# Kernel tuning notes

Hardware: AMD Instinct MI355X
Metric: run time of the kernel (lower is better)

Reference implementation:

```python
import jax, jax.numpy as jnp
import numpy as np

# GNB per-element parameters [s, beta, R, C6] indexed by atomic number Z (rows not listed stay zero)
_ROWS = {
 1:[0.2772,1.7504,3.6516,95.99], 2:[0.2425,2.087,2.1843,40.67], 3:[0.3266,2.3073,1.2711,70.21],
 4:[0.3964,2.8811,3.3497,114.51], 5:[0.3121,2.6366,2.7079,152.36], 6:[0.2455,3.0189,1.8219,184.28],
 7:[0.2743,2.9432,2.4667,482.54], 8:[0.2577,2.7407,2.365,405.57], 9:[0.2791,2.5863,1.5062,218.45],
 10:[0.2378,2.5307,1.8233,174.81], 11:[0.2592,2.5679,1.3974,181.7], 12:[0.3837,2.9613,3.3515,263.02],
 13:[0.3013,3.2377,3.0102,228.1], 14:[0.3202,3.2749,3.1629,359.43], 15:[0.3399,3.7491,3.2554,3222.12],
 16:[0.3215,3.6718,2.9539,2144.49], 17:[0.3071,3.418,3.0368,2072.46], 18:[0.2752,3.3306,2.6598,1357.42],
 19:[0.2264,2.9736,4.0877,1406.65], 20:[0.4015,3.4464,4.1275,1058.36], 21:[0.9388,4.5955,9.7282,11498.73],
 22:[0.6048,3.5334,8.5322,3361.33], 23:[0.3678,3.068,7.2344,2095.91], 24:[0.2848,2.8393,5.3605,1049.31],
 25:[0.355,3.055,3.718,966.27], 26:[0.4406,3.2628,3.6408,1571.36], 27:[0.4124,3.2622,3.4961,1183.59],
 28:[0.3139,2.749,3.5108,787.76], 29:[0.3345,2.9097,3.0537,563.93], 30:[0.3391,2.9024,3.0261,592.91],
 31:[0.3146,3.3924,3.1735,430.82], 32:[0.3327,3.2804,3.1773,812.57], 33:[0.404,3.8757,3.8357,4533.53],
 34:[0.3343,3.8562,3.1109,3440.92], 35:[0.3242,3.7067,3.2122,3859.82], 36:[0.292,3.6457,2.8263,2729.6],
 37:[0.2677,3.4421,2.412,1864.19], 38:[0.3446,3.559,1.894,1175.73], 39:[1.0038,5.7293,11.2061,32141.18],
 40:[0.6146,5.075,6.821,27655.14], 41:[0.4244,3.7156,7.2367,2864.2], 42:[0.4882,3.6853,3.901,3563.45],
 43:[0.4439,3.6987,4.0857,3266.43], 44:[0.4736,3.7826,4.045,3967.23], 45:[0.4039,3.4706,3.4813,2233.82],
 46:[0.3188,3.3433,3.0487,1393.49], 47:[0.2948,3.1186,2.7795,1315.09], 48:[0.3012,3.0853,2.8673,1311.47],
 49:[0.3351,3.5452,3.3339,1460.56], 50:[0.3134,3.2997,3.0086,1662.99], 51:[0.4081,4.1277,3.9919,8089.97],
 52:[0.3585,4.1795,3.4209,6887.05], 53:[0.3574,4.0988,3.5649,8799.32], 54:[0.3134,4.0387,3.0288,6136.5],
 55:[0.2872,3.8468,2.262,3757.31], 56:[0.3788,4.0368,1.3837,2561.18], 57:[1.0851,6.1365,12.171,66580.83],
 72:[0.5577,5.213,6.0791,27593.76], 73:[0.5308,4.7637,5.7661,15364.65], 74:[0.3926,3.6018,3.6366,2734.5],
 75:[0.5351,3.9552,4.241,4801.82], 76:[0.4701,4.0278,4.1348,5685.94], 77:[0.3661,3.6123,3.4213,2786.0],
 78:[0.3411,3.6066,3.2486,2699.79], 79:[0.3164,3.3822,2.9588,2282.6], 80:[0.3047,3.375,2.9381,2476.79],
 81:[0.2802,3.3964,2.7711,2988.7], 82:[0.2682,3.2481,2.5816,2506.63], 83:[0.3876,4.1225,3.785,8916.84],
 84:[0.3679,4.2313,3.5381,8694.22], 85:[0.368,4.2455,3.6985,11821.61], 86:[0.3195,4.1784,3.0551,8410.64],
}
_TAB = np.zeros((87, 4), np.float32)
for _z, _v in _ROWS.items():
    _TAB[_z] = _v
GNB_TABLE = jnp.asarray(_TAB)
C_SP2 = jnp.asarray(np.array([0.2808, 3.0548, 2.2348, 429.69], np.float32))
C_SP3 = jnp.asarray(np.array([0.2455, 3.0189, 1.8219, 184.28], np.float32))
N_CN2 = jnp.asarray(np.array([0.2996, 3.02, 2.6454, 720.18], np.float32))
N_CN3 = jnp.asarray(np.array([0.2743, 2.9432, 2.4667, 482.54], np.float32))

BJ_A1, BJ_A2, BJ_ALPHA = 0.4, 4.0, 14.0
CUTOFF_LR, CUTOFF_START = 10.0, 8.0  # cutoff_start = cutoff_lr - 2.0


def _poly_envelope(x):
    # PolynomialCutoff.calculate_envelope with r_max=1, p=6:
    x6 = x ** 6
    env = 1.0 - 28.0 * x6 + 48.0 * x6 * x - 21.0 * x6 * x * x
    return env * (x < 1.0)


def _gnb_forward(lengths, Z, edge_index):
    n_nodes = Z.shape[0]
    sender, receiver = edge_index[0], edge_index[1]

    # coordination numbers via scatter-add on receiver
    cn = jnp.zeros((n_nodes,), jnp.int32).at[receiver].add(1)

    # species-indexed params with CN-adaptive selection for C and N
    params = GNB_TABLE[Z]  # [N, 4]
    c_params = jnp.where((cn <= 3)[:, None], C_SP2[None, :], C_SP3[None, :])
    n_params = jnp.where((cn <= 2)[:, None], N_CN2[None, :], N_CN3[None, :])
    params = jnp.where((Z == 6)[:, None], c_params, params)
    params = jnp.where((Z == 7)[:, None], n_params, params)

    R_i = params[:, 2]
    C6_i = params[:, 3]

    # geometric-mean combination rules per edge
    C6_ij = jnp.sqrt(C6_i[sender] * C6_i[receiver])
    R_ij = jnp.sqrt(R_i[sender] * R_i[receiver])

    r = lengths
    # BJ damping: f = 1 / (1 + 6 (r/r0)^(-alpha)), r0 = a1 sqrt(R_ij) + a2
    r0 = BJ_A1 * jnp.sqrt(R_ij) + BJ_A2
    f_damp = 1.0 / (1.0 + 6.0 * (r0 / r) ** BJ_ALPHA)

    e_edge = -C6_ij / (R_ij ** 6 + r ** 6) * f_damp

    # long-range polynomial cutoff switching from 1 at cutoff_start to 0 at cutoff_lr
    x = (r - CUTOFF_START) / (CUTOFF_LR - CUTOFF_START)
    env = jnp.where(r < CUTOFF_START, 1.0, _poly_envelope(x))
    e_edge = e_edge * env

    # scatter-sum to atoms; 0.5 to split symmetric pair energy over both directions
    node_energy = jnp.zeros((n_nodes,), e_edge.dtype).at[receiver].add(0.5 * e_edge)
    return node_energy


def setup_inputs() -> dict:
    key = jax.random.key(0)
    k1, k2, k3 = jax.random.split(key, 3)
    n_nodes, n_edges = 100000, 6400000
    Z = jax.random.randint(k1, (n_nodes,), 1, 87, dtype=jnp.int32)
    edge_index = jax.random.randint(k2, (2, n_edges), 0, n_nodes, dtype=jnp.int32)
    lengths = jax.random.uniform(k3, (n_edges,), jnp.float32, 1.0, 10.5)
    return {"Z": Z, "edge_index": edge_index, "lengths": lengths}


def reference(Z, edge_index, lengths):
    return _gnb_forward(lengths, Z, edge_index)
```

## Files before the change

### kernel.cpp

```cpp
#include <hip/hip_runtime.h>


#define B2SHIFT 10
#define B2SIZE  1024
#define TILE    4096
#define SBLK    512
#define ESLICES 32
#define MAXB    128

__device__ __constant__ float2 GNB_RC6[87] = {
    {0.f, 0.f},
    {3.6516f, 95.99f},   {2.1843f, 40.67f},   {1.2711f, 70.21f},
    {3.3497f, 114.51f},  {2.7079f, 152.36f},  {1.8219f, 184.28f},
    {2.4667f, 482.54f},  {2.365f, 405.57f},   {1.5062f, 218.45f},
    {1.8233f, 174.81f},  {1.3974f, 181.7f},   {3.3515f, 263.02f},
    {3.0102f, 228.1f},   {3.1629f, 359.43f},  {3.2554f, 3222.12f},
    {2.9539f, 2144.49f}, {3.0368f, 2072.46f}, {2.6598f, 1357.42f},
    {4.0877f, 1406.65f}, {4.1275f, 1058.36f}, {9.7282f, 11498.73f},
    {8.5322f, 3361.33f}, {7.2344f, 2095.91f}, {5.3605f, 1049.31f},
    {3.718f, 966.27f},   {3.6408f, 1571.36f}, {3.4961f, 1183.59f},
    {3.5108f, 787.76f},  {3.0537f, 563.93f},  {3.0261f, 592.91f},
    {3.1735f, 430.82f},  {3.1773f, 812.57f},  {3.8357f, 4533.53f},
    {3.1109f, 3440.92f}, {3.2122f, 3859.82f}, {2.8263f, 2729.6f},
    {2.412f, 1864.19f},  {1.894f, 1175.73f},  {11.2061f, 32141.18f},
    {6.821f, 27655.14f}, {7.2367f, 2864.2f},  {3.901f, 3563.45f},
    {4.0857f, 3266.43f}, {4.045f, 3967.23f},  {3.4813f, 2233.82f},
    {3.0487f, 1393.49f}, {2.7795f, 1315.09f}, {2.8673f, 1311.47f},
    {3.3339f, 1460.56f}, {3.0086f, 1662.99f}, {3.9919f, 8089.97f},
    {3.4209f, 6887.05f}, {3.5649f, 8799.32f}, {3.0288f, 6136.5f},
    {2.262f, 3757.31f},  {1.3837f, 2561.18f}, {12.171f, 66580.83f},
    {0.f,0.f},{0.f,0.f},{0.f,0.f},{0.f,0.f},{0.f,0.f},{0.f,0.f},{0.f,0.f},
    {0.f,0.f},{0.f,0.f},{0.f,0.f},{0.f,0.f},{0.f,0.f},{0.f,0.f},{0.f,0.f},
    {6.0791f, 27593.76f}, {5.7661f, 15364.65f}, {3.6366f, 2734.5f},
    {4.241f, 4801.82f},   {4.1348f, 5685.94f},  {3.4213f, 2786.0f},
    {3.2486f, 2699.79f},  {2.9588f, 2282.6f},   {2.9381f, 2476.79f},
    {2.7711f, 2988.7f},   {2.5816f, 2506.63f},  {3.785f, 8916.84f},
    {3.5381f, 8694.22f},  {3.6985f, 11821.61f}, {3.0551f, 8410.64f},
};

__global__ void gnb_init(const int* __restrict__ Z, unsigned* __restrict__ isCN,
                         int nw, int n_nodes, int* __restrict__ zp, int zwords) {
    int stride = gridDim.x * blockDim.x;
    int t0 = blockIdx.x * blockDim.x + threadIdx.x;
    for (int i = t0; i < zwords; i += stride) zp[i] = 0;
    for (int w = t0; w < nw; w += stride) {
        unsigned m = 0;
        int base = w << 5;
        int lim = n_nodes - base; if (lim > 32) lim = 32;
        for (int k = 0; k < lim; ++k) {
            int z = Z[base + k];
            if (z == 6 || z == 7) m |= (1u << k);
        }
        isCN[w] = m;
    }
}

__global__ void __launch_bounds__(SBLK)
gnb_scatter(const int* __restrict__ send, const int* __restrict__ recv,
            const float* __restrict__ len, const unsigned* __restrict__ isCN,
            int* __restrict__ cn,
            uint2* __restrict__ buckets, unsigned* __restrict__ cursor,
            uint4* __restrict__ ovrec, unsigned* __restrict__ ocur,
            int n_edges, int cap, unsigned ocap, int NB2) {
    __shared__ unsigned cnt[MAXB];
    __shared__ unsigned pos[MAXB];
    __shared__ unsigned startp[MAXB + 1];
    __shared__ unsigned gbase[MAXB];
    __shared__ uint2 srec[TILE];
    __shared__ unsigned char bmap[TILE];
    const int tid = threadIdx.x;
    const int e0  = blockIdx.x * TILE;

    for (int b = tid; b < MAXB; b += SBLK) { cnt[b] = 0; pos[b] = 0; }
    __syncthreads();

    #pragma unroll
    for (int k = 0; k < 2; ++k) {
        int base = e0 + (k * SBLK + tid) * 4;
        if (base + 3 < n_edges) {
            int4   rv = *(const int4*)(recv + base);
            float4 lv = *(const float4*)(len + base);
            int rr[4] = {rv.x, rv.y, rv.z, rv.w};
            float ll[4] = {lv.x, lv.y, lv.z, lv.w};
            #pragma unroll
            for (int j = 0; j < 4; ++j) {
                unsigned r = (unsigned)rr[j];
                if (ll[j] < 10.0f) atomicAdd(&cnt[r >> B2SHIFT], 1u);
                if ((isCN[r >> 5] >> (r & 31)) & 1u) atomicAdd(&cn[r], 1);
            }
        } else {
            int lim = n_edges - base; if (lim < 0) lim = 0; if (lim > 4) lim = 4;
            for (int j = 0; j < lim; ++j) {
                unsigned r = (unsigned)recv[base + j];
                if (len[base + j] < 10.0f) atomicAdd(&cnt[r >> B2SHIFT], 1u);
                if ((isCN[r >> 5] >> (r & 31)) & 1u) atomicAdd(&cn[r], 1);
            }
        }
    }
    __syncthreads();

    if (tid == 0) {
        unsigned acc = 0;
        for (int b = 0; b < NB2; ++b) { startp[b] = acc; acc += cnt[b]; }
        startp[NB2] = acc;
    }
    __syncthreads();
    if (tid < NB2) gbase[tid] = atomicAdd(&cursor[tid], cnt[tid]);
    __syncthreads();

    #pragma unroll
    for (int k = 0; k < 2; ++k) {
        int base = e0 + (k * SBLK + tid) * 4;
        if (base + 3 < n_edges) {
            int4   sv = *(const int4*)(send + base);
            int4   rv = *(const int4*)(recv + base);
            uint4  lv = *(const uint4*)(len + base);
            int ss[4] = {sv.x, sv.y, sv.z, sv.w};
            int rr[4] = {rv.x, rv.y, rv.z, rv.w};
            unsigned ll[4] = {lv.x, lv.y, lv.z, lv.w};
            #pragma unroll
            for (int j = 0; j < 4; ++j) {
                if (__uint_as_float(ll[j]) >= 10.0f) continue;
                unsigned r = (unsigned)rr[j];
                unsigned b = r >> B2SHIFT;
                unsigned slot = startp[b] + atomicAdd(&pos[b], 1u);
                srec[slot] = make_uint2((unsigned)ss[j] | ((r & (B2SIZE - 1)) << 17), ll[j]);
                bmap[slot] = (unsigned char)b;
            }
        } else {
            int lim = n_edges - base; if (lim < 0) lim = 0; if (lim > 4) lim = 4;
            for (int j = 0; j < lim; ++j) {
                unsigned lbits = ((const unsigned*)len)[base + j];
                if (__uint_as_float(lbits) >= 10.0f) continue;
                unsigned r = (unsigned)recv[base + j];
                unsigned b = r >> B2SHIFT;
                unsigned slot = startp[b] + atomicAdd(&pos[b], 1u);
                srec[slot] = make_uint2((unsigned)send[base + j] | ((r & (B2SIZE - 1)) << 17),
                                        lbits);
                bmap[slot] = (unsigned char)b;
            }
        }
    }
    __syncthreads();

    unsigned total = startp[NB2];
    for (unsigned i = tid; i < total; i += SBLK) {
        unsigned b = bmap[i];
        unsigned g = gbase[b] + (i - startp[b]);
        uint2 rec = srec[i];
        if (g < (unsigned)cap) {
            buckets[(size_t)b * cap + g] = rec;
        } else {
            unsigned o = atomicAdd(ocur, 1u);
            unsigned r = ((unsigned)b << B2SHIFT) | ((rec.x >> 17) & (B2SIZE - 1));
            if (o < ocap) ovrec[o] = make_uint4(r, rec.x & 0x1FFFFu, rec.y, 0u);
        }
    }
}

__global__ void gnb_params(const int* __restrict__ Z, const int* __restrict__ cn,
                           float2* __restrict__ P2, int n_nodes) {
    int i = blockIdx.x * blockDim.x + threadIdx.x;
    if (i >= n_nodes) return;
    int z = Z[i];
    float Rp, C6;
    if (z == 6) {
        if (cn[i] <= 3) { Rp = 2.2348f; C6 = 429.69f; }
        else            { Rp = 1.8219f; C6 = 184.28f; }
    } else if (z == 7) {
        if (cn[i] <= 2) { Rp = 2.6454f; C6 = 720.18f; }
        else            { Rp = 2.4667f; C6 = 482.54f; }
    } else {
        float2 rc = GNB_RC6[z];
        Rp = rc.x; C6 = rc.y;
    }
    P2[i] = make_float2(sqrtf(C6), sqrtf(sqrtf(Rp)));
}

__device__ __forceinline__ float gnb_energy_eval(float2 ps, float2 pr, float rlen) {
    float env;
    if (rlen < 8.0f) {
        env = 1.0f;
    } else {
        float x = (rlen - 8.0f) * 0.5f;
        float x2 = x * x;
        float x6 = x2 * x2 * x2;
        env = 1.0f - 28.0f * x6 + 48.0f * x6 * x - 21.0f * x6 * x2;
    }
    float sR  = ps.y * pr.y;
    float C6  = ps.x * pr.x;
    float Rij = sR * sR;
    float R3  = Rij * Rij * Rij;
    float R6  = R3 * R3;
    float r0  = 0.4f * sR + 4.0f;
    float t   = r0 / rlen;
    float t2 = t * t, t4 = t2 * t2, t8 = t4 * t4;
    float t14 = t8 * t4 * t2;
    float fd = 1.0f / (1.0f + 6.0f * t14);
    float rl2 = rlen * rlen;
    float r6 = rl2 * rl2 * rl2;
    return -0.5f * C6 / (R6 + r6) * fd * env;
}

__global__ void __launch_bounds__(256)
gnb_energy(const uint2* __restrict__ buckets, const unsigned* __restrict__ cursor,
           const float2* __restrict__ P2, float* __restrict__ rep,
           int cap, int n_nodes) {
    __shared__ float  acc[2][B2SIZE + 8];
    __shared__ float2 p2loc[B2SIZE];
    const int b   = blockIdx.x / ESLICES;
    const int sl  = blockIdx.x % ESLICES;
    const int tid = threadIdx.x;
    const int rr  = (tid >> 6) & 1;

    for (int i = tid; i < 2 * (B2SIZE + 8); i += 256) acc[0][i] = 0.0f;
    for (int i = tid; i < B2SIZE; i += 256) {
        int node = (b << B2SHIFT) + i;
        p2loc[i] = (node < n_nodes) ? P2[node] : make_float2(0.f, 0.f);
    }
    __syncthreads();

    unsigned count = cursor[b];
    if (count > (unsigned)cap) count = (unsigned)cap;
    unsigned seg = (count + ESLICES - 1) / ESLICES;
    unsigned st  = (unsigned)sl * seg;
    unsigned en  = st + seg; if (en > count) en = count;

    const uint2* src = buckets + (size_t)b * cap;
    for (unsigned i = st + tid; i < en; i += 256) {
        uint2 rec = src[i];
        unsigned s    = rec.x & 0x1FFFFu;
        unsigned rlow = (rec.x >> 17) & (B2SIZE - 1);
        float e = gnb_energy_eval(P2[s], p2loc[rlow], __uint_as_float(rec.y));
        atomicAdd(&acc[rr][rlow], e);
    }
    __syncthreads();

    float* dst = rep + (size_t)blockIdx.x * B2SIZE;
    for (int i = tid; i < B2SIZE; i += 256) dst[i] = acc[0][i] + acc[1][i];
}

__global__ void gnb_ovf_energy(const uint4* __restrict__ ovrec, const unsigned* __restrict__ ocur,
                               const float2* __restrict__ P2, float* __restrict__ ovf,
                               unsigned ocap) {
    unsigned n = *ocur; if (n > ocap) n = ocap;
    int stride = gridDim.x * blockDim.x;
    for (unsigned i = blockIdx.x * blockDim.x + threadIdx.x; i < n; i += stride) {
        uint4 rec = ovrec[i];
        float rlen = __uint_as_float(rec.z);
        if (rlen >= 10.0f) continue;
        float e = gnb_energy_eval(P2[rec.y], P2[rec.x], rlen);
        atomicAdd(&ovf[rec.x], e);
    }
}

__global__ void gnb_reduce(const float* __restrict__ rep, const float* __restrict__ ovf,
                           float* __restrict__ out, int n_nodes) {
    int i = blockIdx.x * blockDim.x + threadIdx.x;
    if (i >= n_nodes) return;
    int b = i >> B2SHIFT;
    int j = i & (B2SIZE - 1);
    const float* src = rep + ((size_t)b * ESLICES) * B2SIZE + j;
    float sum = ovf[i];
    #pragma unroll
    for (int s = 0; s < ESLICES; ++s) sum += src[(size_t)s * B2SIZE];
    out[i] = sum;
}

extern "C" void kernel_launch(void* const* d_in, const int* in_sizes, int n_in,
                              void* d_out, int out_size, void* d_ws, size_t ws_size,
                              hipStream_t stream) {
    const int*   Z    = (const int*)d_in[0];
    const int*   eidx = (const int*)d_in[1];
    const float* len  = (const float*)d_in[2];
    float*       out  = (float*)d_out;

    const int n_nodes = in_sizes[0];
    const int n_edges = in_sizes[2];
    const int* send = eidx;
    const int* recv = eidx + n_edges;

    const int NB2 = (n_nodes + B2SIZE - 1) >> B2SHIFT;
    const int nw  = (n_nodes + 31) >> 5;
    const int nwp = (nw + 7) & ~7;

    char* ws = (char*)d_ws;
    unsigned* cursor = (unsigned*)ws;
    unsigned* ocur   = (unsigned*)(ws + MAXB * 4);
    int*      cn     = (int*)(ws + (MAXB + 8) * 4);
    float*    ovf    = (float*)(ws + ((size_t)n_nodes + MAXB + 8) * 4);
    float2*   P2     = (float2*)(ws + ((size_t)2 * n_nodes + MAXB + 8) * 4);
    unsigned* isCN   = (unsigned*)(ws + ((size_t)4 * n_nodes + MAXB + 8) * 4);
    float*    rep    = (float*)((char*)isCN + (size_t)nwp * 4);
    size_t rep_w     = (size_t)NB2 * ESLICES * B2SIZE;
    char*     tail   = (char*)rep + rep_w * 4;

    size_t fixed_words = (size_t)4 * n_nodes + MAXB + 8 + nwp + rep_w;
    size_t total_words = ws_size / 4;
    size_t avail = total_words > fixed_words ? total_words - fixed_words : 0;
    size_t ovw = avail / 32;
    unsigned ocap = (unsigned)(ovw / 4);
    long cap = (long)((avail - ovw) / (2 * (size_t)NB2));
    if (cap > n_edges) cap = n_edges;
    if (cap < 0) cap = 0;
    uint4* ovrec   = (uint4*)tail;
    uint2* buckets = (uint2*)(tail + (size_t)ocap * 16);

    const int B = 256;
    int node_blocks = (n_nodes + B - 1) / B;
    int scat_blocks = (n_edges + TILE - 1) / TILE;
    int zero_words  = 2 * n_nodes + MAXB + 8;

    gnb_init<<<256, B, 0, stream>>>(Z, isCN, nw, n_nodes, (int*)ws, zero_words);
    gnb_scatter<<<scat_blocks, SBLK, 0, stream>>>(send, recv, len, isCN, cn, buckets,
                                                  cursor, ovrec, ocur, n_edges,
                                                  (int)cap, ocap, NB2);
    gnb_params<<<node_blocks, B, 0, stream>>>(Z, cn, P2, n_nodes);
    gnb_energy<<<NB2 * ESLICES, B, 0, stream>>>(buckets, cursor, P2, rep, (int)cap, n_nodes);
    gnb_ovf_energy<<<8, B, 0, stream>>>(ovrec, ocur, P2, ovf, ocap);
    gnb_reduce<<<node_blocks, B, 0, stream>>>(rep, ovf, out, n_nodes);
}
```

Baseline: 203.2 us.

## Fuse overflow and reduction into energy kernel, use byte param ids

The per-node float2 parameter array is replaced by a one-byte parameter id per node plus a 91-entry table. The table is built in the init kernel and staged in shared memory by the energy kernel, so the random sender gathers shrink from 8 bytes to 1 byte. The energy kernel now uses 16 slices instead of 32 and reads two records per thread with 128-bit loads. A last-block-done counter per bucket lets the final slice process that bucket's overflow records and write the summed output, which removes the separate overflow and reduce launches. In exchange, the last block of each bucket scans the whole overflow list, and fewer slices per bucket means less parallelism.

```diff
diff --git a/kernel.cpp b/kernel.cpp
--- a/kernel.cpp
+++ b/kernel.cpp
@@ -5,7 +5,7 @@
 #define B2SIZE  1024
 #define TILE    4096
 #define SBLK    512
-#define ESLICES 32
+#define ES      16
 #define MAXB    128
 
 __device__ __constant__ float2 GNB_RC6[87] = {
@@ -39,7 +39,8 @@
 };
 
 __global__ void gnb_init(const int* __restrict__ Z, unsigned* __restrict__ isCN,
-                         int nw, int n_nodes, int* __restrict__ zp, int zwords) {
+                         float2* __restrict__ PT, int nw, int n_nodes,
+                         int* __restrict__ zp, int zwords) {
     int stride = gridDim.x * blockDim.x;
     int t0 = blockIdx.x * blockDim.x + threadIdx.x;
     for (int i = t0; i < zwords; i += stride) zp[i] = 0;
@@ -52,6 +53,15 @@
             if (z == 6 || z == 7) m |= (1u << k);
         }
         isCN[w] = m;
+    }
+    if (t0 < 91) {
+        float R, C6;
+        if      (t0 < 87)  { float2 rc = GNB_RC6[t0]; R = rc.x; C6 = rc.y; }
+        else if (t0 == 87) { R = 2.2348f; C6 = 429.69f; }
+        else if (t0 == 88) { R = 1.8219f; C6 = 184.28f; }
+        else if (t0 == 89) { R = 2.6454f; C6 = 720.18f; }
+        else               { R = 2.4667f; C6 = 482.54f; }
+        PT[t0] = make_float2(sqrtf(C6), sqrtf(sqrtf(R)));
     }
 }
 
@@ -159,22 +169,14 @@
 }
 
 __global__ void gnb_params(const int* __restrict__ Z, const int* __restrict__ cn,
-                           float2* __restrict__ P2, int n_nodes) {
+                           unsigned char* __restrict__ pid, int n_nodes) {
     int i = blockIdx.x * blockDim.x + threadIdx.x;
     if (i >= n_nodes) return;
     int z = Z[i];
-    float Rp, C6;
-    if (z == 6) {
-        if (cn[i] <= 3) { Rp = 2.2348f; C6 = 429.69f; }
-        else            { Rp = 1.8219f; C6 = 184.28f; }
-    } else if (z == 7) {
-        if (cn[i] <= 2) { Rp = 2.6454f; C6 = 720.18f; }
-        else            { Rp = 2.4667f; C6 = 482.54f; }
-    } else {
-        float2 rc = GNB_RC6[z];
-        Rp = rc.x; C6 = rc.y;
-    }
-    P2[i] = make_float2(sqrtf(C6), sqrtf(sqrtf(Rp)));
+    int id = z;
+    if (z == 6)      id = (cn[i] <= 3) ? 87 : 88;
+    else if (z == 7) id = (cn[i] <= 2) ? 89 : 90;
+    pid[i] = (unsigned char)id;
 }
 
 __device__ __forceinline__ float gnb_energy_eval(float2 ps, float2 pr, float rlen) {
@@ -204,67 +206,89 @@
 
 __global__ void __launch_bounds__(256)
 gnb_energy(const uint2* __restrict__ buckets, const unsigned* __restrict__ cursor,
-           const float2* __restrict__ P2, float* __restrict__ rep,
-           int cap, int n_nodes) {
+           const float2* __restrict__ PT, const unsigned char* __restrict__ pid,
+           float* __restrict__ rep, unsigned* __restrict__ done,
+           const uint4* __restrict__ ovrec, const unsigned* __restrict__ ocur,
+           float* __restrict__ out, unsigned ocap, int cap, int n_nodes) {
     __shared__ float  acc[2][B2SIZE + 8];
     __shared__ float2 p2loc[B2SIZE];
-    const int b   = blockIdx.x / ESLICES;
-    const int sl  = blockIdx.x % ESLICES;
+    __shared__ float2 ptab[96];
+    __shared__ unsigned s_old;
     const int tid = threadIdx.x;
+    const int b   = blockIdx.x / ES;
+    const int sl  = blockIdx.x % ES;
     const int rr  = (tid >> 6) & 1;
 
+    if (tid < 91) ptab[tid] = PT[tid];
     for (int i = tid; i < 2 * (B2SIZE + 8); i += 256) acc[0][i] = 0.0f;
     for (int i = tid; i < B2SIZE; i += 256) {
         int node = (b << B2SHIFT) + i;
-        p2loc[i] = (node < n_nodes) ? P2[node] : make_float2(0.f, 0.f);
+        p2loc[i] = (node < n_nodes) ? PT[pid[node]] : make_float2(0.f, 0.f);
     }
     __syncthreads();
 
     unsigned count = cursor[b];
     if (count > (unsigned)cap) count = (unsigned)cap;
-    unsigned seg = (count + ESLICES - 1) / ESLICES;
+    unsigned seg = (((count + ES - 1) / ES) + 1) & ~1u;
     unsigned st  = (unsigned)sl * seg;
     unsigned en  = st + seg; if (en > count) en = count;
 
     const uint2* src = buckets + (size_t)b * cap;
-    for (unsigned i = st + tid; i < en; i += 256) {
-        uint2 rec = src[i];
-        unsigned s    = rec.x & 0x1FFFFu;
-        unsigned rlow = (rec.x >> 17) & (B2SIZE - 1);
-        float e = gnb_energy_eval(P2[s], p2loc[rlow], __uint_as_float(rec.y));
-        atomicAdd(&acc[rr][rlow], e);
+    for (unsigned i = st + 2 * tid; i < en; i += 512) {
+        if (i + 1 < en) {
+            uint4 q = *(const uint4*)(src + i);
+            {
+                unsigned s = q.x & 0x1FFFFu, rl = (q.x >> 17) & (B2SIZE - 1);
+                float e = gnb_energy_eval(ptab[pid[s]], p2loc[rl], __uint_as_float(q.y));
+                atomicAdd(&acc[rr][rl], e);
+            }
+            {
+                unsigned s = q.z & 0x1FFFFu, rl = (q.z >> 17) & (B2SIZE - 1);
+                float e = gnb_energy_eval(ptab[pid[s]], p2loc[rl], __uint_as_float(q.w));
+                atomicAdd(&acc[rr][rl], e);
+            }
+        } else {
+            uint2 rec = src[i];
+            unsigned s = rec.x & 0x1FFFFu, rl = (rec.x >> 17) & (B2SIZE - 1);
+            float e = gnb_energy_eval(ptab[pid[s]], p2loc[rl], __uint_as_float(rec.y));
+            atomicAdd(&acc[rr][rl], e);
+        }
     }
     __syncthreads();
 
     float* dst = rep + (size_t)blockIdx.x * B2SIZE;
     for (int i = tid; i < B2SIZE; i += 256) dst[i] = acc[0][i] + acc[1][i];
-}
-
-__global__ void gnb_ovf_energy(const uint4* __restrict__ ovrec, const unsigned* __restrict__ ocur,
-                               const float2* __restrict__ P2, float* __restrict__ ovf,
-                               unsigned ocap) {
-    unsigned n = *ocur; if (n > ocap) n = ocap;
-    int stride = gridDim.x * blockDim.x;
-    for (unsigned i = blockIdx.x * blockDim.x + threadIdx.x; i < n; i += stride) {
-        uint4 rec = ovrec[i];
-        float rlen = __uint_as_float(rec.z);
-        if (rlen >= 10.0f) continue;
-        float e = gnb_energy_eval(P2[rec.y], P2[rec.x], rlen);
-        atomicAdd(&ovf[rec.x], e);
-    }
-}
-
-__global__ void gnb_reduce(const float* __restrict__ rep, const float* __restrict__ ovf,
-                           float* __restrict__ out, int n_nodes) {
-    int i = blockIdx.x * blockDim.x + threadIdx.x;
-    if (i >= n_nodes) return;
-    int b = i >> B2SHIFT;
-    int j = i & (B2SIZE - 1);
-    const float* src = rep + ((size_t)b * ESLICES) * B2SIZE + j;
-    float sum = ovf[i];
-    #pragma unroll
-    for (int s = 0; s < ESLICES; ++s) sum += src[(size_t)s * B2SIZE];
-    out[i] = sum;
+
+    __threadfence();
+    if (tid == 0) s_old = atomicAdd(&done[b], 1u);
+    __syncthreads();
+    if (s_old != ES - 1) return;
+    __threadfence();
+
+    {
+        unsigned n = *ocur; if (n > ocap) n = ocap;
+        for (unsigned i = tid; i < n; i += 256) {
+            uint4 rec = ovrec[i];
+            if ((int)(rec.x >> B2SHIFT) != b) continue;
+            float rlen = __uint_as_float(rec.z);
+            if (rlen >= 10.0f) continue;
+            float e = gnb_energy_eval(ptab[pid[rec.y]], p2loc[rec.x & (B2SIZE - 1)], rlen);
+            atomicAdd(&acc[0][rec.x & (B2SIZE - 1)], e);
+        }
+    }
+    __syncthreads();
+
+    const float* base = rep + ((size_t)b * ES) * B2SIZE;
+    for (int i = tid; i < B2SIZE; i += 256) {
+        int node = (b << B2SHIFT) + i;
+        if (node >= n_nodes) continue;
+        float sum = acc[0][i] - (acc[0][i] + acc[1][i]);
+        sum = 0.0f;
+        #pragma unroll
+        for (int s = 0; s < ES; ++s) sum += base[(size_t)s * B2SIZE + i];
+        sum += (acc[0][i] + acc[1][i]) - dst[i];
+        out[node] = sum;
+    }
 }
 
 extern "C" void kernel_launch(void* const* d_in, const int* in_sizes, int n_in,
@@ -282,41 +306,49 @@
 
     const int NB2 = (n_nodes + B2SIZE - 1) >> B2SHIFT;
     const int nw  = (n_nodes + 31) >> 5;
-    const int nwp = (nw + 7) & ~7;
+    const size_t nwp   = ((size_t)nw + 3) & ~3ull;
+    const size_t npidw = (((size_t)n_nodes + 3) / 4 + 3) & ~3ull;
+
+    size_t o_done = 136;
+    size_t o_cn   = 264;
+    size_t o_PT   = o_cn + n_nodes;
+    size_t o_isCN = o_PT + 192;
+    size_t o_pid  = o_isCN + nwp;
+    size_t o_rep  = (o_pid + npidw + 3) & ~3ull;
+    size_t rep_w  = (size_t)NB2 * ES * B2SIZE;
+    size_t o_tail = (o_rep + rep_w + 3) & ~3ull;
 
     char* ws = (char*)d_ws;
-    unsigned* cursor = (unsigned*)ws;
-    unsigned* ocur   = (unsigned*)(ws + MAXB * 4);
-    int*      cn     = (int*)(ws + (MAXB + 8) * 4);
-    float*    ovf    = (float*)(ws + ((size_t)n_nodes + MAXB + 8) * 4);
-    float2*   P2     = (float2*)(ws + ((size_t)2 * n_nodes + MAXB + 8) * 4);
-    unsigned* isCN   = (unsigned*)(ws + ((size_t)4 * n_nodes + MAXB + 8) * 4);
-    float*    rep    = (float*)((char*)isCN + (size_t)nwp * 4);
-    size_t rep_w     = (size_t)NB2 * ESLICES * B2SIZE;
-    char*     tail   = (char*)rep + rep_w * 4;
-
-    size_t fixed_words = (size_t)4 * n_nodes + MAXB + 8 + nwp + rep_w;
+    unsigned*      cursor = (unsigned*)ws;
+    unsigned*      ocur   = (unsigned*)(ws + 128 * 4);
+    unsigned*      done   = (unsigned*)(ws + o_done * 4);
+    int*           cn     = (int*)(ws + o_cn * 4);
+    float2*        PT     = (float2*)(ws + o_PT * 4);
+    unsigned*      isCN   = (unsigned*)(ws + o_isCN * 4);
+    unsigned char* pid    = (unsigned char*)(ws + o_pid * 4);
+    float*         rep    = (float*)(ws + o_rep * 4);
+
     size_t total_words = ws_size / 4;
-    size_t avail = total_words > fixed_words ? total_words - fixed_words : 0;
+    size_t avail = total_words > o_tail ? total_words - o_tail : 0;
     size_t ovw = avail / 32;
     unsigned ocap = (unsigned)(ovw / 4);
     long cap = (long)((avail - ovw) / (2 * (size_t)NB2));
     if (cap > n_edges) cap = n_edges;
     if (cap < 0) cap = 0;
-    uint4* ovrec   = (uint4*)tail;
-    uint2* buckets = (uint2*)(tail + (size_t)ocap * 16);
+    cap &= ~1L;
+    uint4* ovrec   = (uint4*)(ws + o_tail * 4);
+    uint2* buckets = (uint2*)(ws + (o_tail + (size_t)ocap * 4) * 4);
 
     const int B = 256;
     int node_blocks = (n_nodes + B - 1) / B;
     int scat_blocks = (n_edges + TILE - 1) / TILE;
-    int zero_words  = 2 * n_nodes + MAXB + 8;
-
-    gnb_init<<<256, B, 0, stream>>>(Z, isCN, nw, n_nodes, (int*)ws, zero_words);
+    int zero_words  = (int)o_PT;
+
+    gnb_init<<<1024, B, 0, stream>>>(Z, isCN, PT, nw, n_nodes, (int*)ws, zero_words);
     gnb_scatter<<<scat_blocks, SBLK, 0, stream>>>(send, recv, len, isCN, cn, buckets,
                                                   cursor, ovrec, ocur, n_edges,
                                                   (int)cap, ocap, NB2);
-    gnb_params<<<node_blocks, B, 0, stream>>>(Z, cn, P2, n_nodes);
-    gnb_energy<<<NB2 * ESLICES, B, 0, stream>>>(buckets, cursor, P2, rep, (int)cap, n_nodes);
-    gnb_ovf_energy<<<8, B, 0, stream>>>(ovrec, ocur, P2, ovf, ocap);
-    gnb_reduce<<<node_blocks, B, 0, stream>>>(rep, ovf, out, n_nodes);
-}
+    gnb_params<<<node_blocks, B, 0, stream>>>(Z, cn, pid, n_nodes);
+    gnb_energy<<<NB2 * ES, B, 0, stream>>>(buckets, cursor, PT, pid, rep, done,
+                                           ovrec, ocur, out, ocap, (int)cap, n_nodes);
+}
```

New measurement: 396.2 us. 95.0% more time.
